# Kernel tuning notes

Hardware: AMD Instinct MI355X
Metric: run time of the kernel (lower is better)

## Reference

```python
import jax, jax.numpy as jnp
import numpy as np
import math

B, H, W, C = 2, 256, 256, 96
HEADS, WS, SHIFT = 6, 8, 4
HD = C // HEADS
N = WS * WS
NW = (H // WS) * (W // WS)
HIDDEN = 2 * C
L = H * W


def _rel_pos_index():
    coords = np.stack(np.meshgrid(np.arange(WS), np.arange(WS), indexing='ij')).reshape(2, -1)
    rel = (coords[:, :, None] - coords[:, None, :]).transpose(1, 2, 0).astype(np.int64)
    rel[:, :, 0] += WS - 1
    rel[:, :, 1] += WS - 1
    rel[:, :, 0] *= 2 * WS - 1
    return rel.sum(-1)  # (N, N)

RPI = jnp.asarray(_rel_pos_index())


def _shift_mask():
    img = np.zeros((H, W), np.float32)
    cnt = 0
    for hs in (slice(0, -WS), slice(-WS, -SHIFT), slice(-SHIFT, None)):
        for ws in (slice(0, -WS), slice(-WS, -SHIFT), slice(-SHIFT, None)):
            img[hs, ws] = cnt
            cnt += 1
    mw = img.reshape(H // WS, WS, W // WS, WS).transpose(0, 2, 1, 3).reshape(-1, N)
    diff = mw[:, None, :] - mw[:, :, None]
    return jnp.asarray(np.where(diff != 0, -100.0, 0.0).astype(np.float32))  # (NW, N, N)

MASK = _shift_mask()


def window_partition(x):  # (b,H,W,c) -> (b*NW,WS,WS,c)
    b = x.shape[0]
    x = x.reshape(b, H // WS, WS, W // WS, WS, -1)
    return x.transpose(0, 1, 3, 2, 4, 5).reshape(b * NW, WS, WS, -1)


def window_reverse(w):  # (b*NW,WS,WS,c) -> (b,H,W,c)
    b = w.shape[0] // NW
    x = w.reshape(b, H // WS, W // WS, WS, WS, -1)
    return x.transpose(0, 1, 3, 2, 4, 5).reshape(b, H, W, -1)


def layernorm(x, g, bt):
    mu = x.mean(-1, keepdims=True)
    var = ((x - mu) ** 2).mean(-1, keepdims=True)
    return (x - mu) / jnp.sqrt(var + 1e-5) * g + bt


def gelu_exact(x):
    return x * 0.5 * (1.0 + jax.lax.erf(x / math.sqrt(2.0)))


def conv3(x, w, b):  # NHWC, HWIO
    return jax.lax.conv_general_dilated(x, w, (1, 1), 'SAME', dimension_numbers=('NHWC', 'HWIO', 'NHWC')) + b


def l2n(x):
    return x / jnp.maximum(jnp.linalg.norm(x, axis=-1, keepdims=True), 1e-12)


def setup_inputs() -> dict:
    key = jax.random.key(0)
    ks = jax.random.split(key, 24)
    s = 0.05
    return {
        'x': jax.random.normal(ks[0], (B, L, C), jnp.float32),
        'ref': jax.random.normal(ks[1], (B, L, C), jnp.float32),
        'norm1_g': jnp.ones((C,), jnp.float32),
        'norm1_b': jnp.zeros((C,), jnp.float32),
        'qkv_w': jax.random.normal(ks[2], (3 * C, C), jnp.float32) * s,
        'qkv_b': jnp.zeros((3 * C,), jnp.float32),
        'logit_scale': jnp.log(10.0) * jnp.ones((HEADS, 1, 1), jnp.float32),
        'gating': jnp.ones((HEADS,), jnp.float32),
        'rpb_table': jax.random.normal(ks[3], ((2 * WS - 1) ** 2, HEADS), jnp.float32) * 0.02,
        'trunk_w': jax.random.normal(ks[4], (4, 3, 3, C, C), jnp.float32) * s,
        'trunk_b': jnp.zeros((4, C), jnp.float32),
        'proj_w': jax.random.normal(ks[5], (C, C), jnp.float32) * s,
        'proj_b': jnp.zeros((C,), jnp.float32),
        'norm2_g': jnp.ones((C,), jnp.float32),
        'norm2_b': jnp.zeros((C,), jnp.float32),
        'fc1_w': jax.random.normal(ks[6], (HIDDEN, C), jnp.float32) * s,
        'fc1_b': jnp.zeros((HIDDEN,), jnp.float32),
        'convm_w': jax.random.normal(ks[7], (3, 3, HIDDEN, HIDDEN), jnp.float32) * s,
        'convm_b': jnp.zeros((HIDDEN,), jnp.float32),
        'fc2_w': jax.random.normal(ks[8], (C, HIDDEN), jnp.float32) * s,
        'fc2_b': jnp.zeros((C,), jnp.float32),
    }


def reference(x, ref, norm1_g, norm1_b, qkv_w, qkv_b, logit_scale, gating, rpb_table,
              trunk_w, trunk_b, proj_w, proj_b, norm2_g, norm2_b,
              fc1_w, fc1_b, convm_w, convm_b, fc2_w, fc2_b):
    shortcut = x
    xi = layernorm(x, norm1_g, norm1_b).reshape(B, H, W, C)
    ri = layernorm(ref, norm1_g, norm1_b).reshape(B, H, W, C)
    xi = jnp.roll(xi, (-SHIFT, -SHIFT), axis=(1, 2))
    ri = jnp.roll(ri, (-SHIFT, -SHIFT), axis=(1, 2))

    def qkv_windows(img):  # (B,H,W,C) -> q,k,v each (B*NW,HEADS,N,HD)
        t = jnp.einsum('bhwc,oc->bhwo', img, qkv_w) + qkv_b  # 1x1 conv
        t = window_partition(t).reshape(B * NW, N, 3, HEADS, HD)
        t = t.transpose(2, 0, 3, 1, 4)
        return t[0], t[1], t[2]

    q, k, v = qkv_windows(xi)
    _, k_r, v_r = qkv_windows(ri)

    ls = jnp.exp(jnp.minimum(logit_scale, math.log(1.0 / 0.01)))  # (HEADS,1,1)
    rpb = rpb_table[RPI.reshape(-1)].reshape(N, N, HEADS).transpose(2, 0, 1)  # (HEADS,N,N)
    qn = l2n(q)
    attn1 = jnp.einsum('bhnd,bhmd->bhnm', qn, l2n(k)) * ls + rpb[None]
    attn2 = jnp.einsum('bhnd,bhmd->bhnm', qn, l2n(k_r)) * ls + rpb[None]
    m = MASK[None, :, None]  # (1,NW,1,N,N)
    attn1 = (attn1.reshape(B, NW, HEADS, N, N) + m).reshape(B * NW, HEADS, N, N)
    attn2 = (attn2.reshape(B, NW, HEADS, N, N) + m).reshape(B * NW, HEADS, N, N)
    a1 = jax.nn.softmax(attn1, axis=-1)
    a2 = jax.nn.softmax(attn2, axis=-1)
    g = jax.nn.sigmoid(gating)[None, :, None, None]
    out = (1.0 - g) * jnp.einsum('bhnm,bhmd->bhnd', a1, v) + g * jnp.einsum('bhnm,bhmd->bhnd', a2, v_r)
    out = out.transpose(0, 2, 1, 3).reshape(B * NW, WS, WS, C)

    img = window_reverse(out)  # (B,H,W,C)
    # trunk branch: 2 residual blocks (conv3-relu-conv3 + skip)
    y = img
    for i in range(2):
        r = conv3(y, trunk_w[2 * i], trunk_b[2 * i])
        r = jax.nn.relu(r)
        r = conv3(r, trunk_w[2 * i + 1], trunk_b[2 * i + 1])
        y = y + r
    y = jnp.einsum('bhwc,oc->bhwo', y, proj_w) + proj_b  # 1x1 proj

    y = jnp.roll(y, (SHIFT, SHIFT), axis=(1, 2)).reshape(B, L, C)
    x = shortcut + y

    # conv-MLP: fc1 -> gelu -> conv3x3+gelu -> fc2
    h = layernorm(x, norm2_g, norm2_b)
    h = gelu_exact(h @ fc1_w.T + fc1_b)
    himg = h.reshape(B, H, W, HIDDEN)
    himg = gelu_exact(conv3(himg, convm_w, convm_b))
    h = himg.reshape(B, L, HIDDEN) @ fc2_w.T + fc2_b
    return x + h
```

## Files before the change

### kernel.cpp

```cpp
#include <hip/hip_runtime.h>
#include <hip/hip_bf16.h>

#define BB 2
#define HH 256
#define WWID 256
#define CC 96
#define NHEADS 6
#define WSZ 8
#define SHIFTV 4
#define HDIM 16
#define NTOK 64
#define HID 192
#define LL 65536

using bf16 = __hip_bfloat16;
typedef short short8v __attribute__((ext_vector_type(8)));
typedef float float4v __attribute__((ext_vector_type(4)));

__device__ __forceinline__ float b2f(bf16 v){ return __bfloat162float(v); }
__device__ __forceinline__ bf16  f2b(float f){ return __float2bfloat16(f); }
__device__ __forceinline__ float blo(unsigned u){ union {unsigned x; float f;} c; c.x = u << 16; return c.f; }
__device__ __forceinline__ float bhi(unsigned u){ union {unsigned x; float f;} c; c.x = u & 0xffff0000u; return c.f; }

__device__ __forceinline__ float dot8(uint4 a, uint4 b, float acc){
  acc += blo(a.x)*blo(b.x); acc += bhi(a.x)*bhi(b.x);
  acc += blo(a.y)*blo(b.y); acc += bhi(a.y)*bhi(b.y);
  acc += blo(a.z)*blo(b.z); acc += bhi(a.z)*bhi(b.z);
  acc += blo(a.w)*blo(b.w); acc += bhi(a.w)*bhi(b.w);
  return acc;
}

__device__ __forceinline__ void gload16(const void* g, void* l){
  __builtin_amdgcn_global_load_lds(
      (const __attribute__((address_space(1))) unsigned int*)g,
      (__attribute__((address_space(3))) unsigned int*)l, 16, 0, 0);
}

__device__ __forceinline__ int swz(int c8, int r){
  return (c8 < 8) ? (c8 ^ (r & 7)) : (8 + ((c8 & 3) ^ ((r >> 1) & 3)));
}

__global__ void detect_kernel(const unsigned* __restrict__ x, int* __restrict__ flag){
  __shared__ int s[256];
  int t = threadIdx.x;
  int cnt = 0;
  #pragma unroll
  for (int i = 0; i < 4; ++i){
    unsigned u = x[t*4 + i];
    unsigned e = (u >> 7) & 0xFFu;
    cnt += (e >= 118u && e <= 130u) ? 1 : 0;
  }
  s[t] = cnt; __syncthreads();
  for (int m = 128; m > 0; m >>= 1){ if (t < m) s[t] += s[t+m]; __syncthreads(); }
  if (t == 0) *flag = (s[0] < 512) ? 1 : 0;
}

struct CvtArgs { const void* src[21]; long cum[22]; long cumP[22]; };

__global__ void cvt_kernel(CvtArgs a, const int* __restrict__ flag,
                           bf16* __restrict__ dst, long totalP){
  long k0 = ((long)blockIdx.x * 256 + threadIdx.x) * 8;
  if (k0 >= totalP) return;
  int lo = 0;
  #pragma unroll
  for (int i = 0; i < 21; ++i) if (k0 >= a.cumP[i+1]) lo = i+1;
  long e = k0 - a.cumP[lo];
  long n = a.cum[lo+1] - a.cum[lo];
  int f = *flag;
  __align__(16) bf16 ob[8];
  if (e + 8 <= n){
    if (f){
      const float* s = (const float*)a.src[lo] + e;
      float4 v0 = *(const float4*)s;
      float4 v1 = *(const float4*)(s + 4);
      ob[0]=f2b(v0.x); ob[1]=f2b(v0.y); ob[2]=f2b(v0.z); ob[3]=f2b(v0.w);
      ob[4]=f2b(v1.x); ob[5]=f2b(v1.y); ob[6]=f2b(v1.z); ob[7]=f2b(v1.w);
    } else {
      *(uint4*)ob = *(const uint4*)((const bf16*)a.src[lo] + e);
    }
  } else {
    #pragma unroll
    for (int j = 0; j < 8; ++j){
      long ee = e + j;
      ob[j] = (ee < n) ? (f ? f2b(((const float*)a.src[lo])[ee])
                            : ((const bf16*)a.src[lo])[ee])
                       : f2b(0.f);
    }
  }
  *(uint4*)&dst[k0] = *(uint4*)ob;
}

__global__ void wprep_kernel(const bf16* __restrict__ w, bf16* __restrict__ out,
                             int CINr, int COUTr, long total){
  long k = (long)blockIdx.x * 256 + threadIdx.x;
  if (k >= total) return;
  int NHr = COUTr / 96, CHr = CINr / 96;
  int region = (int)(k / 10240); int rem = (int)(k - (long)region*10240);
  int gg = rem >> 3, e = rem & 7;
  if (gg >= 1152){ out[k] = f2b(0.f); return; }
  int r = gg / 12, pos = gg - r*12;
  int ch = region % CHr; int t2 = region / CHr;
  int nhh = t2 % NHr; int tap = t2 / NHr;
  int c8 = (pos < 8) ? (pos ^ (r & 7)) : (8 + ((pos & 3) ^ ((r >> 1) & 3)));
  int cin = ch*96 + c8*8 + e;
  int cout = nhh*96 + r;
  out[k] = w[((long)tap*CINr + cin)*COUTr + cout];
}

__global__ __launch_bounds__(256) void ln1_kernel(const bf16* __restrict__ x, const bf16* __restrict__ ref,
                                                  const bf16* __restrict__ g, const bf16* __restrict__ bt,
                                                  bf16* __restrict__ xn, bf16* __restrict__ rn)
{
  int wave = threadIdx.x >> 6, lane = threadIdx.x & 63;
  long row = (long)blockIdx.x * 4 + wave;
  const bf16* src; bf16* dst; long r;
  if (row < (long)BB*LL){ src = x; dst = xn; r = row; }
  else                  { src = ref; dst = rn; r = row - (long)BB*LL; }
  const bf16* p = src + r*CC;
  float v0 = b2f(p[lane]);
  float v1 = (lane < 32) ? b2f(p[64+lane]) : 0.f;
  float s = v0 + v1;
  #pragma unroll
  for (int m = 32; m >= 1; m >>= 1) s += __shfl_xor(s, m, 64);
  float mu = s * (1.f/CC);
  float d0 = v0 - mu, d1 = v1 - mu;
  float ss = d0*d0 + ((lane < 32) ? d1*d1 : 0.f);
  #pragma unroll
  for (int m = 32; m >= 1; m >>= 1) ss += __shfl_xor(ss, m, 64);
  float rstd = rsqrtf(ss * (1.f/CC) + 1e-5f);
  bf16* q = dst + r*CC;
  q[lane] = f2b(d0 * rstd * b2f(g[lane]) + b2f(bt[lane]));
  if (lane < 32) q[64+lane] = f2b(d1 * rstd * b2f(g[64+lane]) + b2f(bt[64+lane]));
}

__global__ __launch_bounds__(256) void ln2_kernel(const bf16* __restrict__ xin,
                                                  const bf16* __restrict__ g, const bf16* __restrict__ bt,
                                                  bf16* __restrict__ out)
{
  int wave = threadIdx.x >> 6, lane = threadIdx.x & 63;
  long r = (long)blockIdx.x * 4 + wave;
  const bf16* p = xin + r*CC;
  float v0 = b2f(p[lane]);
  float v1 = (lane < 32) ? b2f(p[64+lane]) : 0.f;
  float s = v0 + v1;
  #pragma unroll
  for (int m = 32; m >= 1; m >>= 1) s += __shfl_xor(s, m, 64);
  float mu = s * (1.f/CC);
  float d0 = v0 - mu, d1 = v1 - mu;
  float ss = d0*d0 + ((lane < 32) ? d1*d1 : 0.f);
  #pragma unroll
  for (int m = 32; m >= 1; m >>= 1) ss += __shfl_xor(ss, m, 64);
  float rstd = rsqrtf(ss * (1.f/CC) + 1e-5f);
  bf16* q = out + r*CC;
  q[lane] = f2b(d0 * rstd * b2f(g[lane]) + b2f(bt[lane]));
  if (lane < 32) q[64+lane] = f2b(d1 * rstd * b2f(g[64+lane]) + b2f(bt[64+lane]));
}

__global__ __launch_bounds__(256) void attn_kernel(const bf16* __restrict__ xn, const bf16* __restrict__ rn,
                                                   const bf16* __restrict__ qkv_w, const bf16* __restrict__ qkv_b,
                                                   const bf16* __restrict__ lsc, const bf16* __restrict__ gat,
                                                   const bf16* __restrict__ rpbt, bf16* __restrict__ img)
{
  __shared__ __align__(16) bf16 sx[NTOK][104];
  __shared__ __align__(16) bf16 sr[NTOK][104];
  __shared__ __align__(16) bf16 wb[48][104];
  __shared__ float sbias[48];
  __shared__ __align__(16) bf16 qs[NTOK][32];
  __shared__ __align__(16) bf16 ks[NTOK][32];
  __shared__ __align__(16) bf16 krs[NTOK][32];
  __shared__ __align__(16) bf16 vt[16][72];
  __shared__ __align__(16) bf16 vrt[16][72];
  __shared__ __align__(16) bf16 ps[NTOK][72];
  __shared__ float rpbs[225];

  int widx = blockIdx.x;
  int b = widx >> 10, wib = widx & 1023;
  int wh = wib >> 5, ww = wib & 31;
  int tid = threadIdx.x;
  int wv = tid >> 6, lane = tid & 63;
  int ml = lane & 15, quad = lane >> 4;

  for (int idx = tid; idx < NTOK*12; idx += 256){
    int n = idx / 12, c8 = idx - n*12;
    int i = n >> 3, j = n & 7;
    int h0 = (wh*8 + i + SHIFTV) & 255;
    int w0 = (ww*8 + j + SHIFTV) & 255;
    long base = (((long)b*HH + h0)*WWID + w0)*CC + c8*8;
    *(uint4*)&sx[n][c8*8] = *(const uint4*)&xn[base];
    *(uint4*)&sr[n][c8*8] = *(const uint4*)&rn[base];
  }
  for (int idx = tid; idx < 384; idx += 256){
    int arr = idx >> 7, rem = idx & 127;
    int row = rem >> 1, half = rem & 1;
    bf16* bp = (arr == 0) ? &qs[0][0] : (arr == 1) ? &ks[0][0] : &krs[0][0];
    *(uint4*)&bp[row*32 + 16 + half*8] = make_uint4(0,0,0,0);
  }

  for (int h = 0; h < NHEADS; ++h){
    __syncthreads();
    for (int idx = tid; idx < 48*12; idx += 256){
      int rr = idx / 12, c8 = idx - rr*12;
      int o = (rr >> 4)*CC + h*HDIM + (rr & 15);
      *(uint4*)&wb[rr][c8*8] = *(const uint4*)&qkv_w[(long)o*CC + c8*8];
    }
    if (tid < 48){
      int o = (tid >> 4)*CC + h*HDIM + (tid & 15);
      sbias[tid] = b2f(qkv_b[o]);
    }
    if (tid < 225) rpbs[tid] = b2f(rpbt[tid*NHEADS + h]);
    __syncthreads();

    float4v aq0 = {0,0,0,0}, aq1 = {0,0,0,0}, aq2 = {0,0,0,0};
    float4v ar0 = {0,0,0,0}, ar1 = {0,0,0,0};
    {
      int arow = wv*16 + ml;
      #pragma unroll
      for (int kt = 0; kt < 3; ++kt){
        int ko = kt*32 + quad*8;
        short8v ax = *(const short8v*)&sx[arow][ko];
        short8v av = *(const short8v*)&sr[arow][ko];
        short8v b0 = *(const short8v*)&wb[ml][ko];
        short8v b1 = *(const short8v*)&wb[16+ml][ko];
        short8v b2 = *(const short8v*)&wb[32+ml][ko];
        aq0 = __builtin_amdgcn_mfma_f32_16x16x32_bf16(ax, b0, aq0, 0,0,0);
        aq1 = __builtin_amdgcn_mfma_f32_16x16x32_bf16(ax, b1, aq1, 0,0,0);
        aq2 = __builtin_amdgcn_mfma_f32_16x16x32_bf16(ax, b2, aq2, 0,0,0);
        ar0 = __builtin_amdgcn_mfma_f32_16x16x32_bf16(av, b1, ar0, 0,0,0);
        ar1 = __builtin_amdgcn_mfma_f32_16x16x32_bf16(av, b2, ar1, 0,0,0);
      }
    }
    #pragma unroll
    for (int r = 0; r < 4; ++r){
      int tok = wv*16 + quad*4 + r;
      qs[tok][ml]  = f2b(aq0[r] + sbias[ml]);
      ks[tok][ml]  = f2b(aq1[r] + sbias[16+ml]);
      vt[ml][tok]  = f2b(aq2[r] + sbias[32+ml]);
      krs[tok][ml] = f2b(ar0[r] + sbias[16+ml]);
      vrt[ml][tok] = f2b(ar1[r] + sbias[32+ml]);
    }
    __syncthreads();
    if (tid < 192){
      int rr = tid & 63;
      bf16* row = (tid < 64) ? qs[rr] : (tid < 128) ? ks[rr] : krs[rr];
      float s = 0.f;
      #pragma unroll
      for (int d = 0; d < 16; ++d){ float v = b2f(row[d]); s += v*v; }
      float inv = 1.f / fmaxf(sqrtf(s), 1e-12f);
      #pragma unroll
      for (int d = 0; d < 16; ++d) row[d] = f2b(b2f(row[d]) * inv);
    }
    __syncthreads();

    float ls = expf(fminf(b2f(lsc[h]), 4.605170185988091f));
    float gv = b2f(gat[h]);
    float g = 1.f / (1.f + expf(-gv));

    float4v s1[4], s2[4];
    {
      short8v qf = *(const short8v*)&qs[wv*16 + ml][quad*8];
      #pragma unroll
      for (int nt = 0; nt < 4; ++nt){
        short8v kf  = *(const short8v*)&ks[nt*16 + ml][quad*8];
        short8v krf = *(const short8v*)&krs[nt*16 + ml][quad*8];
        float4v z = {0,0,0,0};
        s1[nt] = __builtin_amdgcn_mfma_f32_16x16x32_bf16(qf, kf,  z, 0,0,0);
        s2[nt] = __builtin_amdgcn_mfma_f32_16x16x32_bf16(qf, krf, z, 0,0,0);
      }
    }
    float sv1[4][4], sv2[4][4];
    #pragma unroll
    for (int r = 0; r < 4; ++r){
      int ti = wv*16 + quad*4 + r;
      int iy = ti >> 3, ix = ti & 7;
      int regi = ((wh < 31) ? 0 : (iy < 4 ? 1 : 2))*3 + ((ww < 31) ? 0 : (ix < 4 ? 1 : 2));
      #pragma unroll
      for (int nt = 0; nt < 4; ++nt){
        int tj = nt*16 + ml;
        int jy = tj >> 3, jx = tj & 7;
        int regj = ((wh < 31) ? 0 : (jy < 4 ? 1 : 2))*3 + ((ww < 31) ? 0 : (jx < 4 ? 1 : 2));
        float rp = rpbs[(iy - jy + 7)*15 + (ix - jx + 7)];
        float msk = (regi != regj) ? -100.f : 0.f;
        sv1[nt][r] = s1[nt][r]*ls + rp + msk;
        sv2[nt][r] = s2[nt][r]*ls + rp + msk;
      }
    }
    float f1[4], f2[4];
    #pragma unroll
    for (int r = 0; r < 4; ++r){
      float mx1 = -1e30f, mx2 = -1e30f;
      #pragma unroll
      for (int nt = 0; nt < 4; ++nt){ mx1 = fmaxf(mx1, sv1[nt][r]); mx2 = fmaxf(mx2, sv2[nt][r]); }
      #pragma unroll
      for (int m = 1; m < 16; m <<= 1){ mx1 = fmaxf(mx1, __shfl_xor(mx1, m, 64)); mx2 = fmaxf(mx2, __shfl_xor(mx2, m, 64)); }
      float sm1 = 0.f, sm2 = 0.f;
      #pragma unroll
      for (int nt = 0; nt < 4; ++nt){
        sv1[nt][r] = expf(sv1[nt][r] - mx1); sm1 += sv1[nt][r];
        sv2[nt][r] = expf(sv2[nt][r] - mx2); sm2 += sv2[nt][r];
      }
      #pragma unroll
      for (int m = 1; m < 16; m <<= 1){ sm1 += __shfl_xor(sm1, m, 64); sm2 += __shfl_xor(sm2, m, 64); }
      f1[r] = (1.f - g) / sm1;
      f2[r] = g / sm2;
    }

    #pragma unroll
    for (int r = 0; r < 4; ++r){
      int ti = wv*16 + quad*4 + r;
      #pragma unroll
      for (int nt = 0; nt < 4; ++nt) ps[ti][nt*16 + ml] = f2b(sv1[nt][r] * f1[r]);
    }
    float4v po = {0,0,0,0};
    #pragma unroll
    for (int kt = 0; kt < 2; ++kt){
      short8v pa = *(const short8v*)&ps[wv*16 + ml][kt*32 + quad*8];
      short8v vb = *(const short8v*)&vt[ml][kt*32 + quad*8];
      po = __builtin_amdgcn_mfma_f32_16x16x32_bf16(pa, vb, po, 0,0,0);
    }
    #pragma unroll
    for (int r = 0; r < 4; ++r){
      int ti = wv*16 + quad*4 + r;
      #pragma unroll
      for (int nt = 0; nt < 4; ++nt) ps[ti][nt*16 + ml] = f2b(sv2[nt][r] * f2[r]);
    }
    #pragma unroll
    for (int kt = 0; kt < 2; ++kt){
      short8v pa = *(const short8v*)&ps[wv*16 + ml][kt*32 + quad*8];
      short8v vb = *(const short8v*)&vrt[ml][kt*32 + quad*8];
      po = __builtin_amdgcn_mfma_f32_16x16x32_bf16(pa, vb, po, 0,0,0);
    }
    #pragma unroll
    for (int r = 0; r < 4; ++r){
      int tok = wv*16 + quad*4 + r;
      int hs = wh*8 + (tok >> 3), wsp = ww*8 + (tok & 7);
      img[(((long)b*HH + hs)*WWID + wsp)*CC + h*HDIM + ml] = f2b(po[r]);
    }
  }
}

template<int CIN, int COUT, int MODE>
__global__ __launch_bounds__(256) void convmfma_kernel(const bf16* __restrict__ src,
                                                       const bf16* __restrict__ wtp,
                                                       const bf16* __restrict__ bias,
                                                       const bf16* __restrict__ base,
                                                       bf16* __restrict__ dst)
{
  constexpr int CH = CIN / 96;
  constexpr int NH = COUT / 96;
  constexpr int NS = CH * 9;
  __shared__ __align__(16) bf16 act[180*12*8];
  __shared__ __align__(16) bf16 wl[2][1280*8];

  int tid = threadIdx.x;
  int z = blockIdx.z;
  int bb = z / NH;
  int nh = z % NH;
  int tx0 = blockIdx.x * 16, ty0 = blockIdx.y * 8;
  int wv = tid >> 6, lane = tid & 63;

  auto stage_act = [&](int h){
    for (int idx = tid; idx < 180*12; idx += 256){
      int pp = idx / 12, c8 = idx - pp*12;
      int iy = pp / 18, ix = pp - iy*18;
      int gy = ty0 + iy - 1, gx = tx0 + ix - 1;
      uint4 v = make_uint4(0,0,0,0);
      if ((unsigned)gy < (unsigned)HH && (unsigned)gx < (unsigned)WWID)
        v = *(const uint4*)&src[(((long)bb*HH + gy)*WWID + gx)*CIN + h*96 + c8*8];
      *(uint4*)&act[(pp*12 + swz(c8, pp))*8] = v;
    }
  };
  auto gloadW = [&](int s, int buf){
    int hh = s / 9, tap = s - hh*9;
    int region = (tap*NH + nh)*CH + hh;
    const bf16* g = wtp + (long)region*10240 + (wv*320 + lane)*8;
    bf16* l = &wl[buf][(wv*320)*8];
    #pragma unroll
    for (int i = 0; i < 5; ++i)
      gload16(g + i*512, l + i*512);
  };

  int wm = wv >> 1, wn = wv & 1;
  int ml = lane & 15, quad = lane >> 4;

  float4v acc[4][3];
  #pragma unroll
  for (int nt = 0; nt < 3; ++nt){
    float bv = b2f(bias[nh*96 + wn*48 + nt*16 + ml]);
    #pragma unroll
    for (int mt = 0; mt < 4; ++mt)
      acc[mt][nt] = (float4v){bv, bv, bv, bv};
  }

  int apy = ml >> 3, apx = wm*8 + (ml & 7);

  stage_act(0);
  gloadW(0, 0);
  if (NS > 1) gloadW(1, 1);
  __syncthreads();

  for (int s = 0; s < NS; ++s){
    int h = s / 9, tap = s - h*9;
    int cur = s & 1;
    int dy = tap / 3, dx = tap - dy*3;
    #pragma unroll
    for (int kc = 0; kc < 3; ++kc){
      int posB = (kc < 2) ? ((kc*4 + quad) ^ (ml & 7)) : (8 + (quad ^ ((ml >> 1) & 3)));
      int brow = wn*48 + ml;
      short8v b0 = *(const short8v*)&wl[cur][((brow     )*12 + posB)*8];
      short8v b1 = *(const short8v*)&wl[cur][((brow + 16)*12 + posB)*8];
      short8v b2 = *(const short8v*)&wl[cur][((brow + 32)*12 + posB)*8];
      #pragma unroll
      for (int mt = 0; mt < 4; ++mt){
        int pp = (mt*2 + apy + dy)*18 + apx + dx;
        int posA = (kc < 2) ? ((kc*4 + quad) ^ (pp & 7)) : (8 + (quad ^ ((pp >> 1) & 3)));
        short8v a = *(const short8v*)&act[(pp*12 + posA)*8];
        acc[mt][0] = __builtin_amdgcn_mfma_f32_16x16x32_bf16(a, b0, acc[mt][0], 0, 0, 0);
        acc[mt][1] = __builtin_amdgcn_mfma_f32_16x16x32_bf16(a, b1, acc[mt][1], 0, 0, 0);
        acc[mt][2] = __builtin_amdgcn_mfma_f32_16x16x32_bf16(a, b2, acc[mt][2], 0, 0, 0);
      }
    }
    if (s + 1 == NS) break;
    __syncthreads();
    if (s + 2 < NS) gloadW(s + 2, cur);
    if (tap == 8){
      stage_act(h + 1);
      __syncthreads();
    }
  }

  #pragma unroll
  for (int mt = 0; mt < 4; ++mt){
    #pragma unroll
    for (int r = 0; r < 4; ++r){
      int mrow = quad*4 + r;
      int py = mt*2 + (mrow >> 3), px = wm*8 + (mrow & 7);
      long ob = (((long)bb*HH + ty0+py)*WWID + tx0+px)*COUT + nh*96 + wn*48 + ml;
      #pragma unroll
      for (int nt = 0; nt < 3; ++nt){
        float v = acc[mt][nt][r];
        long o = ob + nt*16;
        if (MODE == 0)      dst[o] = f2b(fmaxf(v, 0.f));
        else if (MODE == 1) dst[o] = f2b(b2f(base[o]) + v);
        else                dst[o] = f2b(0.5f * v * (1.f + erff(v * 0.7071067811865476f)));
      }
    }
  }
}

#define PPITCH (CC+8)
__global__ __launch_bounds__(256) void proj_kernel(const bf16* __restrict__ img, const bf16* __restrict__ pw,
                                                   const bf16* __restrict__ pb, const bf16* __restrict__ xorig,
                                                   bf16* __restrict__ xmid)
{
  __shared__ __align__(16) bf16 rows[64][PPITCH];
  __shared__ __align__(16) bf16 wsm[CC][PPITCH];
  long pix0 = (long)blockIdx.x * 64;
  int tid = threadIdx.x;
  for (int idx = tid; idx < 64*CC; idx += 256){
    int pp = idx / CC, c = idx - pp*CC;
    long pix = pix0 + pp;
    int b = (int)(pix >> 16); int hw = (int)(pix & 65535);
    int h = hw >> 8, wc = hw & 255;
    int sh = (h - SHIFTV) & 255, sw = (wc - SHIFTV) & 255;
    rows[pp][c] = img[(((long)b*HH + sh)*WWID + sw)*CC + c];
  }
  for (int idx = tid; idx < CC*CC; idx += 256){
    int rr = idx / CC, c = idx - rr*CC;
    wsm[rr][c] = pw[idx];
  }
  __syncthreads();
  int ty = tid >> 4, tx = tid & 15;
  int r0 = ty*4;
  float acc[4][6];
  #pragma unroll
  for (int j = 0; j < 6; ++j){
    float bv = b2f(pb[tx + 16*j]);
    #pragma unroll
    for (int i = 0; i < 4; ++i) acc[i][j] = bv;
  }
  for (int kk = 0; kk < 12; ++kk){
    uint4 a0 = ((const uint4*)rows[r0+0])[kk];
    uint4 a1 = ((const uint4*)rows[r0+1])[kk];
    uint4 a2 = ((const uint4*)rows[r0+2])[kk];
    uint4 a3 = ((const uint4*)rows[r0+3])[kk];
    #pragma unroll
    for (int j = 0; j < 6; ++j){
      uint4 wv = ((const uint4*)wsm[tx + 16*j])[kk];
      acc[0][j] = dot8(a0, wv, acc[0][j]);
      acc[1][j] = dot8(a1, wv, acc[1][j]);
      acc[2][j] = dot8(a2, wv, acc[2][j]);
      acc[3][j] = dot8(a3, wv, acc[3][j]);
    }
  }
  #pragma unroll
  for (int i = 0; i < 4; ++i){
    long pix = pix0 + r0 + i;
    #pragma unroll
    for (int j = 0; j < 6; ++j){
      long oi = pix*CC + tx + 16*j;
      xmid[oi] = f2b(b2f(xorig[oi]) + acc[i][j]);
    }
  }
}

__global__ __launch_bounds__(256) void fc1_kernel(const bf16* __restrict__ src, const bf16* __restrict__ w,
                                                  const bf16* __restrict__ bias, bf16* __restrict__ dst)
{
  __shared__ __align__(16) bf16 rows[64][PPITCH];
  __shared__ __align__(16) bf16 wsm[HID][PPITCH];
  long pix0 = (long)blockIdx.x * 64;
  int tid = threadIdx.x;
  for (int idx = tid; idx < 64*CC; idx += 256){
    int pp = idx / CC, c = idx - pp*CC;
    rows[pp][c] = src[(pix0 + pp)*CC + c];
  }
  for (int idx = tid; idx < HID*CC; idx += 256){
    int rr = idx / CC, c = idx - rr*CC;
    wsm[rr][c] = w[idx];
  }
  __syncthreads();
  int ty = tid >> 4, tx = tid & 15;
  int r0 = ty*4;
  float acc[4][12];
  #pragma unroll
  for (int j = 0; j < 12; ++j){
    float bv = b2f(bias[tx + 16*j]);
    #pragma unroll
    for (int i = 0; i < 4; ++i) acc[i][j] = bv;
  }
  for (int kk = 0; kk < 12; ++kk){
    uint4 a0 = ((const uint4*)rows[r0+0])[kk];
    uint4 a1 = ((const uint4*)rows[r0+1])[kk];
    uint4 a2 = ((const uint4*)rows[r0+2])[kk];
    uint4 a3 = ((const uint4*)rows[r0+3])[kk];
    #pragma unroll
    for (int j = 0; j < 12; ++j){
      uint4 wv = ((const uint4*)wsm[tx + 16*j])[kk];
      acc[0][j] = dot8(a0, wv, acc[0][j]);
      acc[1][j] = dot8(a1, wv, acc[1][j]);
      acc[2][j] = dot8(a2, wv, acc[2][j]);
      acc[3][j] = dot8(a3, wv, acc[3][j]);
    }
  }
  #pragma unroll
  for (int i = 0; i < 4; ++i){
    long pix = pix0 + r0 + i;
    #pragma unroll
    for (int j = 0; j < 12; ++j){
      float v = acc[i][j];
      dst[pix*HID + tx + 16*j] = f2b(0.5f * v * (1.f + erff(v * 0.7071067811865476f)));
    }
  }
}

#define FPITCH (HID+8)
__global__ __launch_bounds__(256) void fc2_kernel(const bf16* __restrict__ src, const bf16* __restrict__ w,
                                                  const bf16* __restrict__ bias, const bf16* __restrict__ xmid,
                                                  void* __restrict__ outv, const int* __restrict__ flag)
{
  __shared__ __align__(16) bf16 rows[64][FPITCH];
  __shared__ __align__(16) bf16 wsm[CC][FPITCH];
  long pix0 = (long)blockIdx.x * 64;
  int tid = threadIdx.x;
  for (int idx = tid; idx < 64*HID; idx += 256){
    int pp = idx / HID, c = idx - pp*HID;
    rows[pp][c] = src[(pix0 + pp)*HID + c];
  }
  for (int idx = tid; idx < CC*HID; idx += 256){
    int rr = idx / HID, c = idx - rr*HID;
    wsm[rr][c] = w[idx];
  }
  __syncthreads();
  int ty = tid >> 4, tx = tid & 15;
  int r0 = ty*4;
  float acc[4][6];
  #pragma unroll
  for (int j = 0; j < 6; ++j){
    float bv = b2f(bias[tx + 16*j]);
    #pragma unroll
    for (int i = 0; i < 4; ++i) acc[i][j] = bv;
  }
  for (int kk = 0; kk < 24; ++kk){
    uint4 a0 = ((const uint4*)rows[r0+0])[kk];
    uint4 a1 = ((const uint4*)rows[r0+1])[kk];
    uint4 a2 = ((const uint4*)rows[r0+2])[kk];
    uint4 a3 = ((const uint4*)rows[r0+3])[kk];
    #pragma unroll
    for (int j = 0; j < 6; ++j){
      uint4 wv = ((const uint4*)wsm[tx + 16*j])[kk];
      acc[0][j] = dot8(a0, wv, acc[0][j]);
      acc[1][j] = dot8(a1, wv, acc[1][j]);
      acc[2][j] = dot8(a2, wv, acc[2][j]);
      acc[3][j] = dot8(a3, wv, acc[3][j]);
    }
  }
  int f = *flag;
  #pragma unroll
  for (int i = 0; i < 4; ++i){
    long pix = pix0 + r0 + i;
    #pragma unroll
    for (int j = 0; j < 6; ++j){
      long oi = pix*CC + tx + 16*j;
      float v = b2f(xmid[oi]) + acc[i][j];
      if (f) ((float*)outv)[oi] = v;
      else   ((bf16*)outv)[oi] = f2b(v);
    }
  }
}

extern "C" void kernel_launch(void* const* d_in, const int* in_sizes, int n_in,
                              void* d_out, int out_size, void* d_ws, size_t ws_size,
                              hipStream_t stream)
{
  long cum[22], cumP[22]; cum[0] = 0; cumP[0] = 0;
  for (int i = 0; i < 21; ++i){
    cum[i+1]  = cum[i]  + in_sizes[i];
    cumP[i+1] = cumP[i] + (((long)in_sizes[i] + 7) & ~7L);
  }
  long totalP = cumP[21];

  CvtArgs a;
  for (int i = 0; i < 21; ++i) a.src[i] = d_in[i];
  for (int i = 0; i < 22; ++i){ a.cum[i] = cum[i]; a.cumP[i] = cumP[i]; }

  char* ws = (char*)d_ws;
  int*  flag   = (int*)ws;
  bf16* packed = (bf16*)(ws + 1048576);

  detect_kernel<<<1, 256, 0, stream>>>((const unsigned*)d_in[0], flag);
  cvt_kernel<<<(int)((totalP/8 + 255) / 256), 256, 0, stream>>>(a, flag, packed, totalP);

  #define PP(i) (packed + cumP[i])
  const bf16* xc    = PP(0);
  const bf16* rc    = PP(1);
  const bf16* n1g   = PP(2);
  const bf16* n1b   = PP(3);
  const bf16* qkv_w = PP(4);
  const bf16* qkv_b = PP(5);
  const bf16* lsc   = PP(6);
  const bf16* gat   = PP(7);
  const bf16* rpbt  = PP(8);
  const bf16* tw    = PP(9);
  const bf16* tb    = PP(10);
  const bf16* pw    = PP(11);
  const bf16* pb    = PP(12);
  const bf16* n2g   = PP(13);
  const bf16* n2b   = PP(14);
  const bf16* f1w   = PP(15);
  const bf16* f1b   = PP(16);
  const bf16* cmw   = PP(17);
  const bf16* cmb   = PP(18);
  const bf16* f2w   = PP(19);
  const bf16* f2bp  = PP(20);

  bf16* wtc  = (bf16*)(ws + 52860928);
  bf16* wtm  = (bf16*)(ws + 53598208);
  bf16* xn   = (bf16*)(ws + 54525952);
  bf16* rn   = (bf16*)(ws + 79691776);
  bf16* img  = (bf16*)(ws + 104857600);
  bf16* rtr  = xn;
  bf16* xmid = xn;
  bf16* ln2o = rn;
  bf16* h1   = (bf16*)(ws + 1048576);
  bf16* hc   = rn;

  wprep_kernel<<<1440, 256, 0, stream>>>(tw, wtc, 96, 96, 368640);
  wprep_kernel<<<1440, 256, 0, stream>>>(cmw, wtm, 192, 192, 368640);

  ln1_kernel<<<65536, 256, 0, stream>>>(xc, rc, n1g, n1b, xn, rn);
  attn_kernel<<<2048, 256, 0, stream>>>(xn, rn, qkv_w, qkv_b, lsc, gat, rpbt, img);

  convmfma_kernel<96,96,0><<<dim3(16,32,2), 256, 0, stream>>>(img, wtc + 0L*92160, tb + 0,   nullptr, rtr);
  convmfma_kernel<96,96,1><<<dim3(16,32,2), 256, 0, stream>>>(rtr, wtc + 1L*92160, tb + 96,  img,     img);
  convmfma_kernel<96,96,0><<<dim3(16,32,2), 256, 0, stream>>>(img, wtc + 2L*92160, tb + 192, nullptr, rtr);
  convmfma_kernel<96,96,1><<<dim3(16,32,2), 256, 0, stream>>>(rtr, wtc + 3L*92160, tb + 288, img,     img);

  proj_kernel<<<2048, 256, 0, stream>>>(img, pw, pb, xc, xmid);
  ln2_kernel<<<32768, 256, 0, stream>>>(xmid, n2g, n2b, ln2o);
  fc1_kernel<<<2048, 256, 0, stream>>>(ln2o, f1w, f1b, h1);
  convmfma_kernel<192,192,2><<<dim3(16,32,4), 256, 0, stream>>>(h1, wtm, cmb, nullptr, hc);
  fc2_kernel<<<2048, 256, 0, stream>>>(hc, f2w, f2bp, xmid, d_out, flag);
}
```

Baseline: 900.7 us.

## Transpose attention score layout, fuse L2 norm into registers, alias LDS buffers

The score MFMAs swap their operands so each lane holds a full set of keys for one query row. The softmax max and sum then need only two cross-lane shuffles per value instead of four shuffles per row, and probability stores become packed 4-element writes. The L2 normalization of q/k/k_ref is now done in registers right after the QKV projection, which removes an LDS round trip and one barrier per head. The weight tile and probability buffer share LDS, and the relative-position table is stored as bf16, which cuts shared memory per block to allow higher occupancy. Rounding changes slightly because normalization now happens before the bf16 conversion.

```diff
diff --git a/kernel.cpp b/kernel.cpp
--- a/kernel.cpp
+++ b/kernel.cpp
@@ -163,15 +163,17 @@
 {
   __shared__ __align__(16) bf16 sx[NTOK][104];
   __shared__ __align__(16) bf16 sr[NTOK][104];
-  __shared__ __align__(16) bf16 wb[48][104];
+  __shared__ __align__(16) bf16 wps[48*104];
   __shared__ float sbias[48];
   __shared__ __align__(16) bf16 qs[NTOK][32];
   __shared__ __align__(16) bf16 ks[NTOK][32];
   __shared__ __align__(16) bf16 krs[NTOK][32];
   __shared__ __align__(16) bf16 vt[16][72];
   __shared__ __align__(16) bf16 vrt[16][72];
-  __shared__ __align__(16) bf16 ps[NTOK][72];
-  __shared__ float rpbs[225];
+  __shared__ __align__(16) bf16 rpbs[228];
+
+  bf16 (*wb)[104] = (bf16(*)[104])&wps[0];
+  bf16 (*ps)[72]  = (bf16(*)[72])&wps[0];
 
   int widx = blockIdx.x;
   int b = widx >> 10, wib = widx & 1023;
@@ -207,7 +209,7 @@
       int o = (tid >> 4)*CC + h*HDIM + (tid & 15);
       sbias[tid] = b2f(qkv_b[o]);
     }
-    if (tid < 225) rpbs[tid] = b2f(rpbt[tid*NHEADS + h]);
+    if (tid < 225) rpbs[tid] = rpbt[tid*NHEADS + h];
     __syncthreads();
 
     float4v aq0 = {0,0,0,0}, aq1 = {0,0,0,0}, aq2 = {0,0,0,0};
@@ -229,25 +231,30 @@
         ar1 = __builtin_amdgcn_mfma_f32_16x16x32_bf16(av, b2, ar1, 0,0,0);
       }
     }
-    #pragma unroll
-    for (int r = 0; r < 4; ++r){
-      int tok = wv*16 + quad*4 + r;
-      qs[tok][ml]  = f2b(aq0[r] + sbias[ml]);
-      ks[tok][ml]  = f2b(aq1[r] + sbias[16+ml]);
-      vt[ml][tok]  = f2b(aq2[r] + sbias[32+ml]);
-      krs[tok][ml] = f2b(ar0[r] + sbias[16+ml]);
-      vrt[ml][tok] = f2b(ar1[r] + sbias[32+ml]);
-    }
-    __syncthreads();
-    if (tid < 192){
-      int rr = tid & 63;
-      bf16* row = (tid < 64) ? qs[rr] : (tid < 128) ? ks[rr] : krs[rr];
-      float s = 0.f;
-      #pragma unroll
-      for (int d = 0; d < 16; ++d){ float v = b2f(row[d]); s += v*v; }
-      float inv = 1.f / fmaxf(sqrtf(s), 1e-12f);
-      #pragma unroll
-      for (int d = 0; d < 16; ++d) row[d] = f2b(b2f(row[d]) * inv);
+    {
+      float bq = sbias[ml], bk = sbias[16+ml], bv = sbias[32+ml];
+      #pragma unroll
+      for (int r = 0; r < 4; ++r){
+        float qv  = aq0[r] + bq;
+        float kv  = aq1[r] + bk;
+        float krv = ar0[r] + bk;
+        float sq = qv*qv, sk = kv*kv, skr = krv*krv;
+        #pragma unroll
+        for (int m = 1; m < 16; m <<= 1){
+          sq  += __shfl_xor(sq,  m, 64);
+          sk  += __shfl_xor(sk,  m, 64);
+          skr += __shfl_xor(skr, m, 64);
+        }
+        float iq  = 1.f / fmaxf(sqrtf(sq),  1e-12f);
+        float ik  = 1.f / fmaxf(sqrtf(sk),  1e-12f);
+        float ikr = 1.f / fmaxf(sqrtf(skr), 1e-12f);
+        int tok = wv*16 + quad*4 + r;
+        qs[tok][ml]  = f2b(qv*iq);
+        ks[tok][ml]  = f2b(kv*ik);
+        krs[tok][ml] = f2b(krv*ikr);
+        vt[ml][tok]  = f2b(aq2[r] + bv);
+        vrt[ml][tok] = f2b(ar1[r] + bv);
+      }
     }
     __syncthreads();
 
@@ -263,52 +270,53 @@
         short8v kf  = *(const short8v*)&ks[nt*16 + ml][quad*8];
         short8v krf = *(const short8v*)&krs[nt*16 + ml][quad*8];
         float4v z = {0,0,0,0};
-        s1[nt] = __builtin_amdgcn_mfma_f32_16x16x32_bf16(qf, kf,  z, 0,0,0);
-        s2[nt] = __builtin_amdgcn_mfma_f32_16x16x32_bf16(qf, krf, z, 0,0,0);
+        s1[nt] = __builtin_amdgcn_mfma_f32_16x16x32_bf16(kf,  qf, z, 0,0,0);
+        s2[nt] = __builtin_amdgcn_mfma_f32_16x16x32_bf16(krf, qf, z, 0,0,0);
       }
     }
+    int ti = wv*16 + ml;
+    int iy = ti >> 3, ix = ti & 7;
+    int regi = ((wh < 31) ? 0 : (iy < 4 ? 1 : 2))*3 + ((ww < 31) ? 0 : (ix < 4 ? 1 : 2));
     float sv1[4][4], sv2[4][4];
     #pragma unroll
-    for (int r = 0; r < 4; ++r){
-      int ti = wv*16 + quad*4 + r;
-      int iy = ti >> 3, ix = ti & 7;
-      int regi = ((wh < 31) ? 0 : (iy < 4 ? 1 : 2))*3 + ((ww < 31) ? 0 : (ix < 4 ? 1 : 2));
-      #pragma unroll
-      for (int nt = 0; nt < 4; ++nt){
-        int tj = nt*16 + ml;
+    for (int nt = 0; nt < 4; ++nt){
+      #pragma unroll
+      for (int r = 0; r < 4; ++r){
+        int tj = nt*16 + quad*4 + r;
         int jy = tj >> 3, jx = tj & 7;
         int regj = ((wh < 31) ? 0 : (jy < 4 ? 1 : 2))*3 + ((ww < 31) ? 0 : (jx < 4 ? 1 : 2));
-        float rp = rpbs[(iy - jy + 7)*15 + (ix - jx + 7)];
+        float rp = b2f(rpbs[(iy - jy + 7)*15 + (ix - jx + 7)]);
         float msk = (regi != regj) ? -100.f : 0.f;
         sv1[nt][r] = s1[nt][r]*ls + rp + msk;
         sv2[nt][r] = s2[nt][r]*ls + rp + msk;
       }
     }
-    float f1[4], f2[4];
-    #pragma unroll
-    for (int r = 0; r < 4; ++r){
-      float mx1 = -1e30f, mx2 = -1e30f;
-      #pragma unroll
-      for (int nt = 0; nt < 4; ++nt){ mx1 = fmaxf(mx1, sv1[nt][r]); mx2 = fmaxf(mx2, sv2[nt][r]); }
-      #pragma unroll
-      for (int m = 1; m < 16; m <<= 1){ mx1 = fmaxf(mx1, __shfl_xor(mx1, m, 64)); mx2 = fmaxf(mx2, __shfl_xor(mx2, m, 64)); }
-      float sm1 = 0.f, sm2 = 0.f;
-      #pragma unroll
-      for (int nt = 0; nt < 4; ++nt){
+    float mx1 = -1e30f, mx2 = -1e30f;
+    #pragma unroll
+    for (int nt = 0; nt < 4; ++nt)
+      #pragma unroll
+      for (int r = 0; r < 4; ++r){ mx1 = fmaxf(mx1, sv1[nt][r]); mx2 = fmaxf(mx2, sv2[nt][r]); }
+    mx1 = fmaxf(mx1, __shfl_xor(mx1, 16, 64)); mx1 = fmaxf(mx1, __shfl_xor(mx1, 32, 64));
+    mx2 = fmaxf(mx2, __shfl_xor(mx2, 16, 64)); mx2 = fmaxf(mx2, __shfl_xor(mx2, 32, 64));
+    float sm1 = 0.f, sm2 = 0.f;
+    #pragma unroll
+    for (int nt = 0; nt < 4; ++nt)
+      #pragma unroll
+      for (int r = 0; r < 4; ++r){
         sv1[nt][r] = expf(sv1[nt][r] - mx1); sm1 += sv1[nt][r];
         sv2[nt][r] = expf(sv2[nt][r] - mx2); sm2 += sv2[nt][r];
       }
-      #pragma unroll
-      for (int m = 1; m < 16; m <<= 1){ sm1 += __shfl_xor(sm1, m, 64); sm2 += __shfl_xor(sm2, m, 64); }
-      f1[r] = (1.f - g) / sm1;
-      f2[r] = g / sm2;
-    }
-
-    #pragma unroll
-    for (int r = 0; r < 4; ++r){
-      int ti = wv*16 + quad*4 + r;
-      #pragma unroll
-      for (int nt = 0; nt < 4; ++nt) ps[ti][nt*16 + ml] = f2b(sv1[nt][r] * f1[r]);
+    sm1 += __shfl_xor(sm1, 16, 64); sm1 += __shfl_xor(sm1, 32, 64);
+    sm2 += __shfl_xor(sm2, 16, 64); sm2 += __shfl_xor(sm2, 32, 64);
+    float f1 = (1.f - g) / sm1;
+    float f2 = g / sm2;
+
+    #pragma unroll
+    for (int nt = 0; nt < 4; ++nt){
+      __align__(8) bf16 pk[4];
+      #pragma unroll
+      for (int r = 0; r < 4; ++r) pk[r] = f2b(sv1[nt][r] * f1);
+      *(short4*)&ps[ti][nt*16 + quad*4] = *(short4*)pk;
     }
     float4v po = {0,0,0,0};
     #pragma unroll
@@ -318,10 +326,11 @@
       po = __builtin_amdgcn_mfma_f32_16x16x32_bf16(pa, vb, po, 0,0,0);
     }
     #pragma unroll
-    for (int r = 0; r < 4; ++r){
-      int ti = wv*16 + quad*4 + r;
-      #pragma unroll
-      for (int nt = 0; nt < 4; ++nt) ps[ti][nt*16 + ml] = f2b(sv2[nt][r] * f2[r]);
+    for (int nt = 0; nt < 4; ++nt){
+      __align__(8) bf16 pk[4];
+      #pragma unroll
+      for (int r = 0; r < 4; ++r) pk[r] = f2b(sv2[nt][r] * f2);
+      *(short4*)&ps[ti][nt*16 + quad*4] = *(short4*)pk;
     }
     #pragma unroll
     for (int kt = 0; kt < 2; ++kt){
```

New measurement: 936.9 us. 1.04x slower.
